# Kernel optimization log

Hardware: AMD Instinct MI355X
Metric: run time of the kernel (lower is better)

## Reference

```python
import jax, jax.numpy as jnp
import numpy as np

B, T, E = 2, 2048, 1024   # batch, block_size, emb_d
H, D = 16, 64             # heads, head_size


def setup_inputs() -> dict:
    key = jax.random.key(0)
    ks = jax.random.split(key, 7)
    s = 1.0 / np.sqrt(E)
    inputs = jax.random.normal(ks[0], (B, T, E), dtype=jnp.float32)
    k_w = jax.random.uniform(ks[1], (H, E, D), jnp.float32, -s, s)
    k_b = jax.random.uniform(ks[2], (H, D), jnp.float32, -s, s)
    q_w = jax.random.uniform(ks[3], (H, E, D), jnp.float32, -s, s)
    q_b = jax.random.uniform(ks[4], (H, D), jnp.float32, -s, s)
    v_w = jax.random.uniform(ks[5], (H, E, D), jnp.float32, -s, s)
    v_b = jax.random.uniform(ks[6], (H, D), jnp.float32, -s, s)
    return {"inputs": inputs, "k_w": k_w, "k_b": k_b,
            "q_w": q_w, "q_b": q_b, "v_w": v_w, "v_b": v_b}


def reference(inputs, k_w, k_b, q_w, q_b, v_w, v_b):
    # Per-head linear projections, vectorized over heads: (B,T,E)x(H,E,D)->(B,H,T,D)
    k = jnp.einsum('bte,hed->bhtd', inputs, k_w) + k_b[None, :, None, :]
    q = jnp.einsum('bte,hed->bhtd', inputs, q_w) + q_b[None, :, None, :]
    v = jnp.einsum('bte,hed->bhtd', inputs, v_w) + v_b[None, :, None, :]

    scale = D ** (-0.5)
    # scores: (B,H,Tq,Tk)
    w = jnp.einsum('bhtd,bhsd->bhts', q, k) * scale
    tril = jnp.tril(jnp.ones((T, T), dtype=bool))
    w = jnp.where(tril[None, None, :, :], w, -jnp.inf)
    # NOTE: original torch code does softmax(weights, dim=1) on a (B,T,T)
    # tensor, i.e. over the QUERY axis. Faithfully reproduce: axis=-2 here.
    w = jax.nn.softmax(w, axis=-2)
    out = jnp.einsum('bhts,bhsd->bhtd', w, v)           # (B,H,T,D)
    # concat heads along last dim, head-major order matching torch.cat
    return out.transpose(0, 2, 1, 3).reshape(B, T, H * D)
```

## Files before the change

kernel.cpp:

```cpp
#include <hip/hip_runtime.h>
#include <hip/hip_bf16.h>
#include <math.h>

#define B_ 2
#define T_ 2048
#define E_ 1024
#define H_ 16
#define D_ 64
#define NT_ 32
#define QSCALE 0.180336880f

typedef __attribute__((ext_vector_type(8))) short bf16x8;
typedef __attribute__((ext_vector_type(4))) float f32x4;

#if __has_builtin(__builtin_amdgcn_exp2f)
#define EXP2(x) __builtin_amdgcn_exp2f(x)
#else
#define EXP2(x) exp2f(x)
#endif

__device__ __forceinline__ unsigned short f2bf(float x) {
  union { float f; unsigned u; } v; v.f = x;
  unsigned r = v.u + 0x7FFFu + ((v.u >> 16) & 1u);
  return (unsigned short)(r >> 16);
}
__device__ __forceinline__ unsigned pk2bf(float a, float b) {
  __hip_bfloat162 h = __float22bfloat162_rn(make_float2(a, b));
  union { __hip_bfloat162 h; unsigned u; } c; c.h = h; return c.u;
}

__device__ __forceinline__ void dma8(const unsigned short* g, int gstride,
                                     unsigned short* l, int lane)
{
  const int r = lane >> 3, bg = (lane & 7) ^ (r & 7);
  __builtin_amdgcn_global_load_lds(
      (const __attribute__((address_space(1))) void*)(g + (size_t)r * gstride + bg * 8),
      (__attribute__((address_space(3))) void*)l, 16, 0, 0);
}
__device__ __forceinline__ bf16x8 frag(const unsigned short* tile, int row, int g) {
  return *(const bf16x8*)(tile + row * 64 + (((g ^ row) & 7) << 3));
}

__global__ __launch_bounds__(256) void inpack_kernel(const float* __restrict__ in,
                                                     unsigned short* __restrict__ o) {
  const size_t i = ((size_t)blockIdx.x * 256 + threadIdx.x) * 8;
  float4 f0 = *(const float4*)(in + i);
  float4 f1 = *(const float4*)(in + i + 4);
  unsigned u[4] = { pk2bf(f0.x, f0.y), pk2bf(f0.z, f0.w),
                    pk2bf(f1.x, f1.y), pk2bf(f1.z, f1.w) };
  *(bf16x8*)(o + i) = *(const bf16x8*)u;
}

__global__ __launch_bounds__(256) void wpack_kernel(
    const float* __restrict__ qw, const float* __restrict__ kw, const float* __restrict__ vw,
    unsigned short* __restrict__ qwt, unsigned short* __restrict__ kwt,
    unsigned short* __restrict__ vwt)
{
  __shared__ float s[64][65];
  const int tid = threadIdx.x;
  const int e0 = blockIdx.x * 64, h = blockIdx.y, z = blockIdx.z;
  const float* w = (z == 0) ? qw : (z == 1) ? kw : vw;
  unsigned short* o = (z == 0) ? qwt : (z == 1) ? kwt : vwt;
  {
    const int r = tid >> 2;
    #pragma unroll
    for (int p = 0; p < 4; ++p) {
      const int c = (tid & 3) * 4 + p * 16;
      float4 f = *(const float4*)(w + ((size_t)(h * E_ + e0 + r)) * D_ + c);
      s[r][c] = f.x; s[r][c+1] = f.y; s[r][c+2] = f.z; s[r][c+3] = f.w;
    }
  }
  __syncthreads();
  {
    const int d = tid >> 2, ec = (tid & 3) * 16;
    unsigned short tmp[16];
    #pragma unroll
    for (int j = 0; j < 16; ++j) tmp[j] = f2bf(s[ec + j][d]);
    unsigned short* dst = o + ((size_t)(h * D_ + d)) * E_ + e0 + ec;
    *(bf16x8*)(dst)     = *(const bf16x8*)&tmp[0];
    *(bf16x8*)(dst + 8) = *(const bf16x8*)&tmp[8];
  }
}

__global__ __launch_bounds__(256) void proj_kernel(
    const unsigned short* __restrict__ in16,
    const unsigned short* __restrict__ qwt, const unsigned short* __restrict__ kwt,
    const unsigned short* __restrict__ vwt,
    const float* __restrict__ qb, const float* __restrict__ kb, const float* __restrict__ vb,
    unsigned short* __restrict__ qo, unsigned short* __restrict__ ko,
    unsigned short* __restrict__ vt)
{
  __shared__ __align__(16) unsigned short in_s[2][128 * 64];
  __shared__ __align__(16) unsigned short w_s[2][3][64 * 64];
  const int tid = threadIdx.x;
  const int lane = tid & 63, wv = tid >> 6;
  const int l15 = lane & 15, quad = lane >> 4;
  const int t0 = blockIdx.x * 128, h = blockIdx.y, b = blockIdx.z;
  const int bh = b * H_ + h;
  const unsigned short* wts[3] = { qwt, kwt, vwt };

  f32x4 acc[3][2][4];
  #pragma unroll
  for (int x = 0; x < 3; ++x)
    #pragma unroll
    for (int s = 0; s < 2; ++s)
      #pragma unroll
      for (int nb = 0; nb < 4; ++nb) acc[x][s][nb] = (f32x4){0.f, 0.f, 0.f, 0.f};

#define PROJ_STAGE(e0_, bi_)                                                      \
  {                                                                               \
    const unsigned short* gin = in16 + ((size_t)(b * T_ + t0)) * E_ + (e0_);      \
    _Pragma("unroll")                                                             \
    for (int p = 0; p < 4; ++p) {                                                 \
      const int br = wv * 32 + p * 8;                                             \
      dma8(gin + (size_t)br * E_, E_, &in_s[bi_][br * 64], lane);                 \
    }                                                                             \
    _Pragma("unroll")                                                             \
    for (int j = 0; j < 6; ++j) {                                                 \
      const int idx = wv * 6 + j;                                                 \
      const int x = idx >> 3, br = (idx & 7) * 8;                                 \
      dma8(wts[x] + ((size_t)(h * D_ + br)) * E_ + (e0_), E_,                     \
           &w_s[bi_][x][br * 64], lane);                                          \
    }                                                                             \
  }

  PROJ_STAGE(0, 0);
  __syncthreads();
  for (int e = 0; e < 16; ++e) {
    const int bi = e & 1;
    if (e < 15) PROJ_STAGE((e + 1) * 64, bi ^ 1);
    const unsigned short* is = in_s[bi];
    #pragma unroll
    for (int kk = 0; kk < 2; ++kk) {
      const int g0 = kk * 4 + quad;
      bf16x8 a0 = frag(is, wv * 32 + l15, g0);
      bf16x8 a1 = frag(is, wv * 32 + 16 + l15, g0);
      #pragma unroll
      for (int x = 0; x < 3; ++x) {
        const unsigned short* ws = w_s[bi][x];
        #pragma unroll
        for (int nb = 0; nb < 4; ++nb) {
          bf16x8 bfr = frag(ws, nb * 16 + l15, g0);
          if (x < 2) {
            acc[x][0][nb] = __builtin_amdgcn_mfma_f32_16x16x32_bf16(bfr, a0, acc[x][0][nb], 0, 0, 0);
            acc[x][1][nb] = __builtin_amdgcn_mfma_f32_16x16x32_bf16(bfr, a1, acc[x][1][nb], 0, 0, 0);
          } else {
            acc[x][0][nb] = __builtin_amdgcn_mfma_f32_16x16x32_bf16(a0, bfr, acc[x][0][nb], 0, 0, 0);
            acc[x][1][nb] = __builtin_amdgcn_mfma_f32_16x16x32_bf16(a1, bfr, acc[x][1][nb], 0, 0, 0);
          }
        }
      }
    }
    __syncthreads();
  }
#undef PROJ_STAGE

  const size_t obase = (size_t)bh * T_;
  #pragma unroll
  for (int x = 0; x < 2; ++x) {
    const float scl = (x == 0) ? QSCALE : 1.0f;
    const float* bias = (x == 0) ? qb : kb;
    unsigned short* outp = (x == 0) ? qo : ko;
    #pragma unroll
    for (int nb = 0; nb < 4; ++nb) {
      float bias4[4];
      *(float4*)bias4 = *(const float4*)&bias[h * D_ + nb * 16 + quad * 4];
      #pragma unroll
      for (int s = 0; s < 2; ++s) {
        const int t = t0 + wv * 32 + s * 16 + l15;
        unsigned short pk[4];
        #pragma unroll
        for (int r = 0; r < 4; ++r) pk[r] = f2bf((acc[x][s][nb][r] + bias4[r]) * scl);
        *(ushort4*)(outp + (obase + t) * D_ + nb * 16 + quad * 4) = *(const ushort4*)pk;
      }
    }
  }
  #pragma unroll
  for (int nb = 0; nb < 4; ++nb) {
    const int d = nb * 16 + l15;
    const float bvv = vb[h * D_ + d];
    #pragma unroll
    for (int s = 0; s < 2; ++s) {
      const int t = t0 + wv * 32 + s * 16 + quad * 4;
      unsigned short pk[4];
      #pragma unroll
      for (int r = 0; r < 4; ++r) pk[r] = f2bf(acc[2][s][nb][r] + bvv);
      *(ushort4*)(vt + ((size_t)(bh * D_ + d)) * T_ + t) = *(const ushort4*)pk;
    }
  }
}

__global__ __launch_bounds__(256, 6) void stats_kernel(
    const unsigned short* __restrict__ q, const unsigned short* __restrict__ k,
    float* __restrict__ lg)
{
  __shared__ __align__(16) unsigned short q_s[2][64 * 64];
  __shared__ float red[4][64];
  const int tid = threadIdx.x;
  const int lane = tid & 63, wv = tid >> 6;
  const int l15 = lane & 15, quad = lane >> 4;
  const int h = blockIdx.x, b = blockIdx.y, sa = blockIdx.z;
  const int bh = b * H_ + h;
  const int s0 = sa * 64;
  const unsigned short* qbase = q + (size_t)bh * T_ * 64;

  bf16x8 kf[4][2];
  #pragma unroll
  for (int nb = 0; nb < 4; ++nb)
    #pragma unroll
    for (int kk = 0; kk < 2; ++kk)
      kf[nb][kk] = *(const bf16x8*)(k + ((size_t)(bh * T_ + s0 + nb * 16 + l15)) * 64
                                      + kk * 32 + quad * 8);

  #pragma unroll
  for (int pp = 0; pp < 2; ++pp) {
    const int br = wv * 16 + pp * 8;
    dma8(qbase + (size_t)(sa * 64 + br) * 64, 64, &q_s[0][br * 64], lane);
  }
  __syncthreads();

  float lsum[4] = {0.f, 0.f, 0.f, 0.f};

  for (int tt = sa, i = 0; tt < NT_; ++tt, ++i) {
    const int bi = i & 1;
    if (tt + 1 < NT_) {
      #pragma unroll
      for (int pp = 0; pp < 2; ++pp) {
        const int br = wv * 16 + pp * 8;
        dma8(qbase + (size_t)((tt + 1) * 64 + br) * 64, 64, &q_s[bi ^ 1][br * 64], lane);
      }
    }
    bf16x8 a0 = frag(q_s[bi], wv * 16 + l15, quad);
    bf16x8 a1 = frag(q_s[bi], wv * 16 + l15, 4 + quad);
    f32x4 sacc[4];
    #pragma unroll
    for (int nb = 0; nb < 4; ++nb) sacc[nb] = (f32x4){0.f, 0.f, 0.f, 0.f};
    #pragma unroll
    for (int nb = 0; nb < 4; ++nb) {
      sacc[nb] = __builtin_amdgcn_mfma_f32_16x16x32_bf16(a0, kf[nb][0], sacc[nb], 0, 0, 0);
      sacc[nb] = __builtin_amdgcn_mfma_f32_16x16x32_bf16(a1, kf[nb][1], sacc[nb], 0, 0, 0);
    }
    if (tt == sa) {
      const int tbase = tt * 64 + wv * 16 + quad * 4;
      #pragma unroll
      for (int nb = 0; nb < 4; ++nb) {
        const int s = s0 + nb * 16 + l15;
        #pragma unroll
        for (int r = 0; r < 4; ++r)
          lsum[nb] += (tbase + r >= s) ? EXP2(sacc[nb][r]) : 0.f;
      }
    } else {
      #pragma unroll
      for (int nb = 0; nb < 4; ++nb)
        #pragma unroll
        for (int r = 0; r < 4; ++r) lsum[nb] += EXP2(sacc[nb][r]);
    }
    __syncthreads();
  }
  #pragma unroll
  for (int nb = 0; nb < 4; ++nb) {
    lsum[nb] += __shfl_xor(lsum[nb], 16);
    lsum[nb] += __shfl_xor(lsum[nb], 32);
  }
  if (lane < 16) {
    #pragma unroll
    for (int nb = 0; nb < 4; ++nb) red[wv][nb * 16 + lane] = lsum[nb];
  }
  __syncthreads();
  if (tid < 64) {
    const float L = red[0][tid] + red[1][tid] + red[2][tid] + red[3][tid];
    lg[(size_t)bh * T_ + s0 + tid] = -__log2f(L);
  }
}

__global__ __launch_bounds__(256, 6) void out_kernel(
    const unsigned short* __restrict__ q, const unsigned short* __restrict__ k,
    const unsigned short* __restrict__ vt, const float* __restrict__ lg,
    float* __restrict__ out)
{
  __shared__ __align__(16) unsigned short k_s[64 * 64];
  __shared__ __align__(16) unsigned short vt_s[64 * 64];
  __shared__ __align__(16) unsigned short u_s[4][16][72];
  __shared__ float lg_sh[64];
  const int tid = threadIdx.x;
  const int lane = tid & 63, wv = tid >> 6;
  const int l15 = lane & 15, quad = lane >> 4;
  const int h = blockIdx.x, b = blockIdx.y, jt = 31 - blockIdx.z;
  const int bh = b * H_ + h;
  const int t0 = jt * 64;
  const unsigned short* kbase = k + (size_t)bh * T_ * 64;
  const unsigned short* vbase = vt + (size_t)bh * D_ * T_;
  const float* lgbase = lg + (size_t)bh * T_;

  const unsigned short* qrow = q + (size_t)(bh * T_ + t0 + wv * 16 + l15) * 64;
  bf16x8 qf0 = *(const bf16x8*)(qrow + quad * 8);
  bf16x8 qf1 = *(const bf16x8*)(qrow + 32 + quad * 8);

  f32x4 oacc[4];
  #pragma unroll
  for (int nb = 0; nb < 4; ++nb) oacc[nb] = (f32x4){0.f, 0.f, 0.f, 0.f};

  unsigned short* urow = &u_s[wv][l15][0];
  const int tcol = t0 + wv * 16 + l15;

  for (int st = 0; st <= jt; ++st) {
    const int s0 = st * 64;
    __syncthreads();
    #pragma unroll
    for (int pp = 0; pp < 2; ++pp) {
      const int br = wv * 16 + pp * 8;
      dma8(kbase + (size_t)(s0 + br) * 64, 64, &k_s[br * 64], lane);
      dma8(vbase + (size_t)br * T_ + s0, T_, &vt_s[br * 64], lane);
    }
    if (tid < 64) lg_sh[tid] = lgbase[s0 + tid];
    __syncthreads();
    f32x4 sacc[4];
    #pragma unroll
    for (int mb = 0; mb < 4; ++mb) {
      float lg4[4];
      *(float4*)lg4 = *(const float4*)&lg_sh[mb * 16 + quad * 4];
      sacc[mb] = (f32x4){lg4[0], lg4[1], lg4[2], lg4[3]};
    }
    #pragma unroll
    for (int mb = 0; mb < 4; ++mb) {
      bf16x8 ka0 = frag(k_s, mb * 16 + l15, quad);
      bf16x8 ka1 = frag(k_s, mb * 16 + l15, 4 + quad);
      sacc[mb] = __builtin_amdgcn_mfma_f32_16x16x32_bf16(ka0, qf0, sacc[mb], 0, 0, 0);
      sacc[mb] = __builtin_amdgcn_mfma_f32_16x16x32_bf16(ka1, qf1, sacc[mb], 0, 0, 0);
    }
    if (st == jt) {
      #pragma unroll
      for (int mb = 0; mb < 4; ++mb) {
        const int sbase = s0 + mb * 16 + quad * 4;
        float uu[4] = { EXP2(sacc[mb][0]), EXP2(sacc[mb][1]),
                        EXP2(sacc[mb][2]), EXP2(sacc[mb][3]) };
        #pragma unroll
        for (int r = 0; r < 4; ++r) if (tcol < sbase + r) uu[r] = 0.f;
        *(uint2*)(urow + mb * 16 + quad * 4) =
            make_uint2(pk2bf(uu[0], uu[1]), pk2bf(uu[2], uu[3]));
      }
    } else {
      #pragma unroll
      for (int mb = 0; mb < 4; ++mb) {
        float uu[4] = { EXP2(sacc[mb][0]), EXP2(sacc[mb][1]),
                        EXP2(sacc[mb][2]), EXP2(sacc[mb][3]) };
        *(uint2*)(urow + mb * 16 + quad * 4) =
            make_uint2(pk2bf(uu[0], uu[1]), pk2bf(uu[2], uu[3]));
      }
    }
    #pragma unroll
    for (int kk = 0; kk < 2; ++kk) {
      bf16x8 ua = *(const bf16x8*)(urow + kk * 32 + quad * 8);
      #pragma unroll
      for (int nb = 0; nb < 4; ++nb)
        oacc[nb] = __builtin_amdgcn_mfma_f32_16x16x32_bf16(
            frag(vt_s, nb * 16 + l15, kk * 4 + quad), ua, oacc[nb], 0, 0, 0);
    }
  }
  float* orow = out + ((size_t)(b * T_ + t0 + wv * 16 + l15)) * (H_ * D_) + h * D_;
  #pragma unroll
  for (int nb = 0; nb < 4; ++nb) {
    float o4[4] = { oacc[nb][0], oacc[nb][1], oacc[nb][2], oacc[nb][3] };
    *(float4*)(orow + nb * 16 + quad * 4) = *(const float4*)o4;
  }
}

extern "C" void kernel_launch(void* const* d_in, const int* in_sizes, int n_in,
                              void* d_out, int out_size, void* d_ws, size_t ws_size,
                              hipStream_t stream) {
  const float* in = (const float*)d_in[0];
  const float* kw = (const float*)d_in[1];
  const float* kb = (const float*)d_in[2];
  const float* qw = (const float*)d_in[3];
  const float* qb = (const float*)d_in[4];
  const float* vw = (const float*)d_in[5];
  const float* vb = (const float*)d_in[6];
  float* out = (float*)d_out;

  unsigned short* p = (unsigned short*)d_ws;
  const size_t inz = (size_t)B_ * T_ * E_;
  const size_t wz  = (size_t)H_ * D_ * E_;
  const size_t qz  = (size_t)B_ * H_ * T_ * D_;
  unsigned short* in16 = p;            p += inz;
  unsigned short* qwt  = p;            p += wz;
  unsigned short* kwt  = p;            p += wz;
  unsigned short* vwt  = p;            p += wz;
  unsigned short* q16  = p;            p += qz;
  unsigned short* k16  = p;            p += qz;
  unsigned short* vtb  = p;            p += qz;
  float* lgbuf = (float*)p;

  dim3 blk(256);
  inpack_kernel<<<dim3(inz / 2048), blk, 0, stream>>>(in, in16);
  wpack_kernel <<<dim3(E_ / 64, H_, 3), blk, 0, stream>>>(qw, kw, vw, qwt, kwt, vwt);
  proj_kernel  <<<dim3(T_ / 128, H_, B_), blk, 0, stream>>>(in16, qwt, kwt, vwt,
                                                            qb, kb, vb, q16, k16, vtb);
  stats_kernel <<<dim3(H_, B_, NT_), blk, 0, stream>>>(q16, k16, lgbuf);
  out_kernel   <<<dim3(H_, B_, NT_), blk, 0, stream>>>(q16, k16, vtb, lgbuf, out);
}
```

Measured before the change: 180.2 us.

## Pair causal tiles per block and double-buffer K/V loads in out kernel

Stats and output kernels now each handle a pair of tiles, one short and one long along the causal triangle (p and 31-p), so every block does the same amount of work and shared K/V tiles are reused across the two query tiles. The out kernel also double-buffers the K and V^T tiles and the log-sum values, prefetching the next tile while computing the current one, and hoists the K fragments out of the per-query-tile loop. Grids shrink to 16 in z, halving the block count. More registers per thread and the dropped occupancy hint may lower occupancy, and fewer blocks (512) may underfill the CUs.

```diff
diff --git a/kernel.cpp b/kernel.cpp
--- a/kernel.cpp
+++ b/kernel.cpp
@@ -190,27 +190,32 @@
   }
 }
 
-__global__ __launch_bounds__(256, 6) void stats_kernel(
+__global__ __launch_bounds__(256) void stats_kernel(
     const unsigned short* __restrict__ q, const unsigned short* __restrict__ k,
     float* __restrict__ lg)
 {
   __shared__ __align__(16) unsigned short q_s[2][64 * 64];
-  __shared__ float red[4][64];
+  __shared__ float red[4][2][64];
   const int tid = threadIdx.x;
   const int lane = tid & 63, wv = tid >> 6;
   const int l15 = lane & 15, quad = lane >> 4;
-  const int h = blockIdx.x, b = blockIdx.y, sa = blockIdx.z;
+  const int h = blockIdx.x, b = blockIdx.y, p = blockIdx.z;
+  const int sa = p, sb = 31 - p;
+  const int s0a = sa * 64, s0b = sb * 64;
   const int bh = b * H_ + h;
-  const int s0 = sa * 64;
   const unsigned short* qbase = q + (size_t)bh * T_ * 64;
 
-  bf16x8 kf[4][2];
-  #pragma unroll
-  for (int nb = 0; nb < 4; ++nb)
-    #pragma unroll
-    for (int kk = 0; kk < 2; ++kk)
-      kf[nb][kk] = *(const bf16x8*)(k + ((size_t)(bh * T_ + s0 + nb * 16 + l15)) * 64
-                                      + kk * 32 + quad * 8);
+  bf16x8 kf[2][4][2];
+  #pragma unroll
+  for (int tl = 0; tl < 2; ++tl) {
+    const int s0 = tl ? s0b : s0a;
+    #pragma unroll
+    for (int nb = 0; nb < 4; ++nb)
+      #pragma unroll
+      for (int kk = 0; kk < 2; ++kk)
+        kf[tl][nb][kk] = *(const bf16x8*)(k + ((size_t)(bh * T_ + s0 + nb * 16 + l15)) * 64
+                                            + kk * 32 + quad * 8);
+  }
 
   #pragma unroll
   for (int pp = 0; pp < 2; ++pp) {
@@ -219,7 +224,11 @@
   }
   __syncthreads();
 
-  float lsum[4] = {0.f, 0.f, 0.f, 0.f};
+  float lsum[2][4];
+  #pragma unroll
+  for (int tl = 0; tl < 2; ++tl)
+    #pragma unroll
+    for (int nb = 0; nb < 4; ++nb) lsum[tl][nb] = 0.f;
 
   for (int tt = sa, i = 0; tt < NT_; ++tt, ++i) {
     const int bi = i & 1;
@@ -232,136 +241,206 @@
     }
     bf16x8 a0 = frag(q_s[bi], wv * 16 + l15, quad);
     bf16x8 a1 = frag(q_s[bi], wv * 16 + l15, 4 + quad);
-    f32x4 sacc[4];
-    #pragma unroll
-    for (int nb = 0; nb < 4; ++nb) sacc[nb] = (f32x4){0.f, 0.f, 0.f, 0.f};
+    {
+      f32x4 sacc[4];
+      #pragma unroll
+      for (int nb = 0; nb < 4; ++nb) sacc[nb] = (f32x4){0.f, 0.f, 0.f, 0.f};
+      #pragma unroll
+      for (int nb = 0; nb < 4; ++nb) {
+        sacc[nb] = __builtin_amdgcn_mfma_f32_16x16x32_bf16(a0, kf[0][nb][0], sacc[nb], 0, 0, 0);
+        sacc[nb] = __builtin_amdgcn_mfma_f32_16x16x32_bf16(a1, kf[0][nb][1], sacc[nb], 0, 0, 0);
+      }
+      if (tt == sa) {
+        const int tbase = tt * 64 + wv * 16 + quad * 4;
+        #pragma unroll
+        for (int nb = 0; nb < 4; ++nb) {
+          const int s = s0a + nb * 16 + l15;
+          #pragma unroll
+          for (int r = 0; r < 4; ++r)
+            lsum[0][nb] += (tbase + r >= s) ? EXP2(sacc[nb][r]) : 0.f;
+        }
+      } else {
+        #pragma unroll
+        for (int nb = 0; nb < 4; ++nb)
+          #pragma unroll
+          for (int r = 0; r < 4; ++r) lsum[0][nb] += EXP2(sacc[nb][r]);
+      }
+    }
+    if (tt >= sb) {
+      f32x4 sacc[4];
+      #pragma unroll
+      for (int nb = 0; nb < 4; ++nb) sacc[nb] = (f32x4){0.f, 0.f, 0.f, 0.f};
+      #pragma unroll
+      for (int nb = 0; nb < 4; ++nb) {
+        sacc[nb] = __builtin_amdgcn_mfma_f32_16x16x32_bf16(a0, kf[1][nb][0], sacc[nb], 0, 0, 0);
+        sacc[nb] = __builtin_amdgcn_mfma_f32_16x16x32_bf16(a1, kf[1][nb][1], sacc[nb], 0, 0, 0);
+      }
+      if (tt == sb) {
+        const int tbase = tt * 64 + wv * 16 + quad * 4;
+        #pragma unroll
+        for (int nb = 0; nb < 4; ++nb) {
+          const int s = s0b + nb * 16 + l15;
+          #pragma unroll
+          for (int r = 0; r < 4; ++r)
+            lsum[1][nb] += (tbase + r >= s) ? EXP2(sacc[nb][r]) : 0.f;
+        }
+      } else {
+        #pragma unroll
+        for (int nb = 0; nb < 4; ++nb)
+          #pragma unroll
+          for (int r = 0; r < 4; ++r) lsum[1][nb] += EXP2(sacc[nb][r]);
+      }
+    }
+    __syncthreads();
+  }
+  #pragma unroll
+  for (int tl = 0; tl < 2; ++tl)
     #pragma unroll
     for (int nb = 0; nb < 4; ++nb) {
-      sacc[nb] = __builtin_amdgcn_mfma_f32_16x16x32_bf16(a0, kf[nb][0], sacc[nb], 0, 0, 0);
-      sacc[nb] = __builtin_amdgcn_mfma_f32_16x16x32_bf16(a1, kf[nb][1], sacc[nb], 0, 0, 0);
-    }
-    if (tt == sa) {
-      const int tbase = tt * 64 + wv * 16 + quad * 4;
-      #pragma unroll
-      for (int nb = 0; nb < 4; ++nb) {
-        const int s = s0 + nb * 16 + l15;
-        #pragma unroll
-        for (int r = 0; r < 4; ++r)
-          lsum[nb] += (tbase + r >= s) ? EXP2(sacc[nb][r]) : 0.f;
-      }
-    } else {
-      #pragma unroll
-      for (int nb = 0; nb < 4; ++nb)
-        #pragma unroll
-        for (int r = 0; r < 4; ++r) lsum[nb] += EXP2(sacc[nb][r]);
-    }
-    __syncthreads();
-  }
-  #pragma unroll
-  for (int nb = 0; nb < 4; ++nb) {
-    lsum[nb] += __shfl_xor(lsum[nb], 16);
-    lsum[nb] += __shfl_xor(lsum[nb], 32);
-  }
+      lsum[tl][nb] += __shfl_xor(lsum[tl][nb], 16);
+      lsum[tl][nb] += __shfl_xor(lsum[tl][nb], 32);
+    }
   if (lane < 16) {
     #pragma unroll
-    for (int nb = 0; nb < 4; ++nb) red[wv][nb * 16 + lane] = lsum[nb];
+    for (int tl = 0; tl < 2; ++tl)
+      #pragma unroll
+      for (int nb = 0; nb < 4; ++nb) red[wv][tl][nb * 16 + lane] = lsum[tl][nb];
   }
   __syncthreads();
-  if (tid < 64) {
-    const float L = red[0][tid] + red[1][tid] + red[2][tid] + red[3][tid];
-    lg[(size_t)bh * T_ + s0 + tid] = -__log2f(L);
-  }
-}
-
-__global__ __launch_bounds__(256, 6) void out_kernel(
+  if (tid < 128) {
+    const int tl = tid >> 6, sL = tid & 63;
+    const float L = red[0][tl][sL] + red[1][tl][sL] + red[2][tl][sL] + red[3][tl][sL];
+    lg[(size_t)bh * T_ + (tl ? s0b : s0a) + sL] = -__log2f(L);
+  }
+}
+
+__global__ __launch_bounds__(256) void out_kernel(
     const unsigned short* __restrict__ q, const unsigned short* __restrict__ k,
     const unsigned short* __restrict__ vt, const float* __restrict__ lg,
     float* __restrict__ out)
 {
-  __shared__ __align__(16) unsigned short k_s[64 * 64];
-  __shared__ __align__(16) unsigned short vt_s[64 * 64];
+  __shared__ __align__(16) unsigned short k_s[2][64 * 64];
+  __shared__ __align__(16) unsigned short vt_s[2][64 * 64];
   __shared__ __align__(16) unsigned short u_s[4][16][72];
-  __shared__ float lg_sh[64];
+  __shared__ float lg_sh[2][64];
   const int tid = threadIdx.x;
   const int lane = tid & 63, wv = tid >> 6;
   const int l15 = lane & 15, quad = lane >> 4;
-  const int h = blockIdx.x, b = blockIdx.y, jt = 31 - blockIdx.z;
+  const int h = blockIdx.x, b = blockIdx.y, p = blockIdx.z;
+  const int ja = p, jb = 31 - p;
+  const int t0a = ja * 64, t0b = jb * 64;
   const int bh = b * H_ + h;
-  const int t0 = jt * 64;
   const unsigned short* kbase = k + (size_t)bh * T_ * 64;
   const unsigned short* vbase = vt + (size_t)bh * D_ * T_;
   const float* lgbase = lg + (size_t)bh * T_;
 
-  const unsigned short* qrow = q + (size_t)(bh * T_ + t0 + wv * 16 + l15) * 64;
-  bf16x8 qf0 = *(const bf16x8*)(qrow + quad * 8);
-  bf16x8 qf1 = *(const bf16x8*)(qrow + 32 + quad * 8);
-
-  f32x4 oacc[4];
-  #pragma unroll
-  for (int nb = 0; nb < 4; ++nb) oacc[nb] = (f32x4){0.f, 0.f, 0.f, 0.f};
+  bf16x8 qf[2][2];
+  #pragma unroll
+  for (int ti = 0; ti < 2; ++ti) {
+    const unsigned short* qrow =
+        q + (size_t)(bh * T_ + (ti ? t0b : t0a) + wv * 16 + l15) * 64;
+    qf[ti][0] = *(const bf16x8*)(qrow + quad * 8);
+    qf[ti][1] = *(const bf16x8*)(qrow + 32 + quad * 8);
+  }
+
+  #pragma unroll
+  for (int pp = 0; pp < 2; ++pp) {
+    const int br = wv * 16 + pp * 8;
+    dma8(kbase + (size_t)br * 64, 64, &k_s[0][br * 64], lane);
+    dma8(vbase + (size_t)br * T_, T_, &vt_s[0][br * 64], lane);
+  }
+  if (tid < 64) lg_sh[0][tid] = lgbase[tid];
+  __syncthreads();
+
+  f32x4 oacc[2][4];
+  #pragma unroll
+  for (int ti = 0; ti < 2; ++ti)
+    #pragma unroll
+    for (int nb = 0; nb < 4; ++nb) oacc[ti][nb] = (f32x4){0.f, 0.f, 0.f, 0.f};
 
   unsigned short* urow = &u_s[wv][l15][0];
-  const int tcol = t0 + wv * 16 + l15;
-
-  for (int st = 0; st <= jt; ++st) {
+  const int tcola = t0a + wv * 16 + l15;
+  const int tcolb = t0b + wv * 16 + l15;
+
+  for (int st = 0; st <= jb; ++st) {
+    const int bi = st & 1;
+    if (st < jb) {
+      const int s1 = (st + 1) * 64;
+      #pragma unroll
+      for (int pp = 0; pp < 2; ++pp) {
+        const int br = wv * 16 + pp * 8;
+        dma8(kbase + (size_t)(s1 + br) * 64, 64, &k_s[bi ^ 1][br * 64], lane);
+        dma8(vbase + (size_t)br * T_ + s1, T_, &vt_s[bi ^ 1][br * 64], lane);
+      }
+      if (tid < 64) lg_sh[bi ^ 1][tid] = lgbase[s1 + tid];
+    }
     const int s0 = st * 64;
+    const unsigned short* ks = k_s[bi];
+    const unsigned short* vs = vt_s[bi];
+    const float* lgb = lg_sh[bi];
+    bf16x8 ka[4][2];
+    #pragma unroll
+    for (int mb = 0; mb < 4; ++mb) {
+      ka[mb][0] = frag(ks, mb * 16 + l15, quad);
+      ka[mb][1] = frag(ks, mb * 16 + l15, 4 + quad);
+    }
+    #pragma unroll
+    for (int ti = 0; ti < 2; ++ti) {
+      if (ti == 0 && st > ja) continue;
+      const int jt = ti ? jb : ja;
+      const int tcol = ti ? tcolb : tcola;
+      f32x4 sacc[4];
+      #pragma unroll
+      for (int mb = 0; mb < 4; ++mb) {
+        float lg4[4];
+        *(float4*)lg4 = *(const float4*)&lgb[mb * 16 + quad * 4];
+        sacc[mb] = (f32x4){lg4[0], lg4[1], lg4[2], lg4[3]};
+      }
+      #pragma unroll
+      for (int mb = 0; mb < 4; ++mb) {
+        sacc[mb] = __builtin_amdgcn_mfma_f32_16x16x32_bf16(ka[mb][0], qf[ti][0], sacc[mb], 0, 0, 0);
+        sacc[mb] = __builtin_amdgcn_mfma_f32_16x16x32_bf16(ka[mb][1], qf[ti][1], sacc[mb], 0, 0, 0);
+      }
+      if (st == jt) {
+        #pragma unroll
+        for (int mb = 0; mb < 4; ++mb) {
+          const int sbase = s0 + mb * 16 + quad * 4;
+          float uu[4] = { EXP2(sacc[mb][0]), EXP2(sacc[mb][1]),
+                          EXP2(sacc[mb][2]), EXP2(sacc[mb][3]) };
+          #pragma unroll
+          for (int r = 0; r < 4; ++r) if (tcol < sbase + r) uu[r] = 0.f;
+          *(uint2*)(urow + mb * 16 + quad * 4) =
+              make_uint2(pk2bf(uu[0], uu[1]), pk2bf(uu[2], uu[3]));
+        }
+      } else {
+        #pragma unroll
+        for (int mb = 0; mb < 4; ++mb) {
+          float uu[4] = { EXP2(sacc[mb][0]), EXP2(sacc[mb][1]),
+                          EXP2(sacc[mb][2]), EXP2(sacc[mb][3]) };
+          *(uint2*)(urow + mb * 16 + quad * 4) =
+              make_uint2(pk2bf(uu[0], uu[1]), pk2bf(uu[2], uu[3]));
+        }
+      }
+      #pragma unroll
+      for (int kk = 0; kk < 2; ++kk) {
+        bf16x8 ua = *(const bf16x8*)(urow + kk * 32 + quad * 8);
+        #pragma unroll
+        for (int nb = 0; nb < 4; ++nb)
+          oacc[ti][nb] = __builtin_amdgcn_mfma_f32_16x16x32_bf16(
+              frag(vs, nb * 16 + l15, kk * 4 + quad), ua, oacc[ti][nb], 0, 0, 0);
+      }
+    }
     __syncthreads();
-    #pragma unroll
-    for (int pp = 0; pp < 2; ++pp) {
-      const int br = wv * 16 + pp * 8;
-      dma8(kbase + (size_t)(s0 + br) * 64, 64, &k_s[br * 64], lane);
-      dma8(vbase + (size_t)br * T_ + s0, T_, &vt_s[br * 64], lane);
-    }
-    if (tid < 64) lg_sh[tid] = lgbase[s0 + tid];
-    __syncthreads();
-    f32x4 sacc[4];
-    #pragma unroll
-    for (int mb = 0; mb < 4; ++mb) {
-      float lg4[4];
-      *(float4*)lg4 = *(const float4*)&lg_sh[mb * 16 + quad * 4];
-      sacc[mb] = (f32x4){lg4[0], lg4[1], lg4[2], lg4[3]};
-    }
-    #pragma unroll
-    for (int mb = 0; mb < 4; ++mb) {
-      bf16x8 ka0 = frag(k_s, mb * 16 + l15, quad);
-      bf16x8 ka1 = frag(k_s, mb * 16 + l15, 4 + quad);
-      sacc[mb] = __builtin_amdgcn_mfma_f32_16x16x32_bf16(ka0, qf0, sacc[mb], 0, 0, 0);
-      sacc[mb] = __builtin_amdgcn_mfma_f32_16x16x32_bf16(ka1, qf1, sacc[mb], 0, 0, 0);
-    }
-    if (st == jt) {
-      #pragma unroll
-      for (int mb = 0; mb < 4; ++mb) {
-        const int sbase = s0 + mb * 16 + quad * 4;
-        float uu[4] = { EXP2(sacc[mb][0]), EXP2(sacc[mb][1]),
-                        EXP2(sacc[mb][2]), EXP2(sacc[mb][3]) };
-        #pragma unroll
-        for (int r = 0; r < 4; ++r) if (tcol < sbase + r) uu[r] = 0.f;
-        *(uint2*)(urow + mb * 16 + quad * 4) =
-            make_uint2(pk2bf(uu[0], uu[1]), pk2bf(uu[2], uu[3]));
-      }
-    } else {
-      #pragma unroll
-      for (int mb = 0; mb < 4; ++mb) {
-        float uu[4] = { EXP2(sacc[mb][0]), EXP2(sacc[mb][1]),
-                        EXP2(sacc[mb][2]), EXP2(sacc[mb][3]) };
-        *(uint2*)(urow + mb * 16 + quad * 4) =
-            make_uint2(pk2bf(uu[0], uu[1]), pk2bf(uu[2], uu[3]));
-      }
-    }
-    #pragma unroll
-    for (int kk = 0; kk < 2; ++kk) {
-      bf16x8 ua = *(const bf16x8*)(urow + kk * 32 + quad * 8);
-      #pragma unroll
-      for (int nb = 0; nb < 4; ++nb)
-        oacc[nb] = __builtin_amdgcn_mfma_f32_16x16x32_bf16(
-            frag(vt_s, nb * 16 + l15, kk * 4 + quad), ua, oacc[nb], 0, 0, 0);
-    }
-  }
-  float* orow = out + ((size_t)(b * T_ + t0 + wv * 16 + l15)) * (H_ * D_) + h * D_;
-  #pragma unroll
-  for (int nb = 0; nb < 4; ++nb) {
-    float o4[4] = { oacc[nb][0], oacc[nb][1], oacc[nb][2], oacc[nb][3] };
-    *(float4*)(orow + nb * 16 + quad * 4) = *(const float4*)o4;
+  }
+  #pragma unroll
+  for (int ti = 0; ti < 2; ++ti) {
+    const int t0 = ti ? t0b : t0a;
+    float* orow = out + ((size_t)(b * T_ + t0 + wv * 16 + l15)) * (H_ * D_) + h * D_;
+    #pragma unroll
+    for (int nb = 0; nb < 4; ++nb) {
+      float o4[4] = { oacc[ti][nb][0], oacc[ti][nb][1], oacc[ti][nb][2], oacc[ti][nb][3] };
+      *(float4*)(orow + nb * 16 + quad * 4) = *(const float4*)o4;
+    }
   }
 }
 
@@ -395,6 +474,6 @@
   wpack_kernel <<<dim3(E_ / 64, H_, 3), blk, 0, stream>>>(qw, kw, vw, qwt, kwt, vwt);
   proj_kernel  <<<dim3(T_ / 128, H_, B_), blk, 0, stream>>>(in16, qwt, kwt, vwt,
                                                             qb, kb, vb, q16, k16, vtb);
-  stats_kernel <<<dim3(H_, B_, NT_), blk, 0, stream>>>(q16, k16, lgbuf);
-  out_kernel   <<<dim3(H_, B_, NT_), blk, 0, stream>>>(q16, k16, vtb, lgbuf, out);
-}
+  stats_kernel <<<dim3(H_, B_, 16), blk, 0, stream>>>(q16, k16, lgbuf);
+  out_kernel   <<<dim3(H_, B_, 16), blk, 0, stream>>>(q16, k16, vtb, lgbuf, out);
+}
```

Result: slower. 184.4 us (+2.3%).
